# Optimization experiments

Hardware: AMD Instinct MI355X
Metric: run time of the kernel (lower is better)

Reference implementation:

```python
import jax, jax.numpy as jnp
import numpy as np
from jax.ops import segment_sum

B = 4096      # graphs per side (= batch of triples)
NPG = 32      # nodes per graph
N = B * NPG   # total nodes per batched graph
EPG = 128     # edges per graph
E = B * EPG   # total edges per batched graph
D = 256       # emb_dim
D4 = D // 4   # gnn1 out dim


def setup_inputs() -> dict:
    key = jax.random.key(0)
    ks = jax.random.split(key, 16)
    base = jnp.repeat(jnp.arange(B, dtype=jnp.int32) * NPG, EPG)  # graph offsets per edge
    def edges(k1, k2):
        s = base + jax.random.randint(k1, (E,), 0, NPG, dtype=jnp.int32)
        d = base + jax.random.randint(k2, (E,), 0, NPG, dtype=jnp.int32)
        return s, d
    subj_src, subj_dst = edges(ks[0], ks[1])
    obj_src, obj_dst = edges(ks[2], ks[3])
    node_graph_ids = jnp.repeat(jnp.arange(B, dtype=jnp.int32), NPG)
    # negative sampling indices (precomputed randomness, as in _sample_batch_negative_triples)
    head_or_tail = jax.random.randint(ks[4], (B,), 0, 2, dtype=jnp.int32)
    random_rows = jax.random.permutation(ks[5], B).astype(jnp.int32)
    ar = jnp.arange(B, dtype=jnp.int32)
    corrupt_hidx = jnp.where(head_or_tail == 1, random_rows, ar)
    corrupt_tidx = jnp.where(head_or_tail == 0, random_rows, ar)
    s = 0.02
    p = lambda k, sh: jax.random.normal(k, sh, dtype=jnp.float32) * s
    return {
        "subj_node_embs": jax.random.normal(ks[6], (N, D), dtype=jnp.float32),
        "obj_node_embs": jax.random.normal(ks[7], (N, D), dtype=jnp.float32),
        "rel_tok_embs": jax.random.normal(ks[8], (B, D), dtype=jnp.float32),
        "subj_src": subj_src, "subj_dst": subj_dst,
        "obj_src": obj_src, "obj_dst": obj_dst,
        "node_graph_ids": node_graph_ids,
        "corrupt_hidx": corrupt_hidx, "corrupt_tidx": corrupt_tidx,
        "WO1": p(ks[9], (D4, D)), "bO1": jnp.zeros((D4,), jnp.float32),
        "WI1": p(ks[10], (D4, D)), "bI1": jnp.zeros((D4,), jnp.float32),
        "WO2": p(ks[11], (D, D4)), "bO2": jnp.zeros((D,), jnp.float32),
        "WI2": p(ks[12], (D, D4)), "bI2": jnp.zeros((D,), jnp.float32),
        "relW": p(ks[13], (D, D)), "relb": jnp.zeros((D,), jnp.float32),
    }


def _mean_agg(h, idx_from, idx_to, n):
    # mean over edges (idx_from -> idx_to) of h[idx_from], per destination node; 0 for isolated
    deg = segment_sum(jnp.ones((idx_from.shape[0],), h.dtype), idx_to, num_segments=n)
    s = segment_sum(jnp.take(h, idx_from, axis=0), idx_to, num_segments=n)
    return s / jnp.maximum(deg, 1.0)[:, None]


def _compgcn(src, dst, h, WO, bO, WI, bI):
    n = h.shape[0]
    ho = _mean_agg(h, src, dst, n)   # forward graph: mean of in-neighbor sources
    hi = _mean_agg(h, dst, src, n)   # reversed graph: mean of out-neighbor targets
    return (ho @ WO.T + bO) + (hi @ WI.T + bI)


def _graph_emb(src, dst, node_embs, gids, WO1, bO1, WI1, bI1, WO2, bO2, WI2, bI2):
    hn = jax.nn.relu(_compgcn(src, dst, node_embs, WO1, bO1, WI1, bI1))
    hn = jax.nn.relu(_compgcn(src, dst, hn, WO2, bO2, WI2, bI2))
    # mean readout per graph
    cnt = segment_sum(jnp.ones((hn.shape[0],), hn.dtype), gids, num_segments=B)
    return segment_sum(hn, gids, num_segments=B) / cnt[:, None]


def _dist(h, r, t):
    return jnp.linalg.norm(h + r - t, ord=2, axis=1)


def reference(subj_node_embs, obj_node_embs, rel_tok_embs,
              subj_src, subj_dst, obj_src, obj_dst, node_graph_ids,
              corrupt_hidx, corrupt_tidx,
              WO1, bO1, WI1, bI1, WO2, bO2, WI2, bI2, relW, relb):
    h_embs = _graph_emb(subj_src, subj_dst, subj_node_embs, node_graph_ids,
                        WO1, bO1, WI1, bI1, WO2, bO2, WI2, bI2)
    t_embs = _graph_emb(obj_src, obj_dst, obj_node_embs, node_graph_ids,
                        WO1, bO1, WI1, bI1, WO2, bO2, WI2, bI2)
    r_embs = jax.nn.relu(rel_tok_embs @ relW.T + relb)
    pos_scores = _dist(h_embs, r_embs, t_embs)
    neg_scores = _dist(h_embs[corrupt_hidx], r_embs, t_embs[corrupt_tidx])
    return pos_scores, neg_scores
```

## Files before the change

### kernel.cpp

```cpp
#include <hip/hip_runtime.h>
#include <hip/hip_bf16.h>

#define BGR 4096
#define DIM 256
#define NGPB 4
#define HS  257

typedef __bf16 bf16x8 __attribute__((ext_vector_type(8)));
typedef __bf16 bf16x4 __attribute__((ext_vector_type(4)));
typedef float  f32x4  __attribute__((ext_vector_type(4)));

typedef const __attribute__((address_space(1))) unsigned int* gas_u32p;
typedef __attribute__((address_space(3))) unsigned int* las_u32p;

__device__ __forceinline__ unsigned short f2b(float f) {
  unsigned u = __builtin_bit_cast(unsigned, f);
  u = (u + 0x7FFFu + ((u >> 16) & 1u)) >> 16;
  return (unsigned short)u;
}

__device__ __forceinline__ bf16x8 cvt8(float4 a, float4 b) {
  bf16x8 r;
  r[0] = (__bf16)a.x; r[1] = (__bf16)a.y; r[2] = (__bf16)a.z; r[3] = (__bf16)a.w;
  r[4] = (__bf16)b.x; r[5] = (__bf16)b.y; r[6] = (__bf16)b.z; r[7] = (__bf16)b.w;
  return r;
}
__device__ __forceinline__ bf16x4 cvt4(f32x4 c) {
  bf16x4 r;
  r[0] = (__bf16)c[0]; r[1] = (__bf16)c[1]; r[2] = (__bf16)c[2]; r[3] = (__bf16)c[3];
  return r;
}

__global__ void wcvt_kernel(
    const float* __restrict__ WO1, const float* __restrict__ WI1,
    const float* __restrict__ WO2, const float* __restrict__ WI2,
    const float* __restrict__ bO1, const float* __restrict__ bI1,
    const float* __restrict__ bO2, const float* __restrict__ bI2,
    unsigned short* __restrict__ W1b, unsigned short* __restrict__ W2b,
    float* __restrict__ b1, float* __restrict__ b2)
{
  const int i = blockIdx.x * 256 + threadIdx.x;
  { int j = i >> 8, k = i & 255;
    float v = (j < 64) ? WO1[j * 256 + k] : WI1[(j - 64) * 256 + k];
    W1b[i] = f2b(v); }
  { int j = i >> 7, k = i & 127;
    float v = (k < 64) ? WO2[j * 64 + k] : WI2[j * 64 + (k - 64)];
    W2b[i] = f2b(v); }
  if (i < 64)  b1[i] = bO1[i] + bI1[i];
  if (i < 256) b2[i] = bO2[i] + bI2[i];
}

__global__ __launch_bounds__(256)
__attribute__((amdgpu_waves_per_eu(1, 2)))
void gemm0_kernel(
    const float* __restrict__ subj, const float* __restrict__ obj,
    const unsigned short* __restrict__ W1b, unsigned short* __restrict__ Yt)
{
  __shared__ __align__(16) float S[2][32 * 256];
  const int t = threadIdx.x, w = t >> 6, l = t & 63;
  const int ln16 = l & 15, kg = l >> 4;
  const int gid0 = blockIdx.x * NGPB;

  {
    const int gid = gid0;
    const float* Eg = ((gid >> 12) ? obj : subj) + (size_t)(gid & (BGR - 1)) * 32 * DIM;
    #pragma unroll
    for (int i = 0; i < 8; i++) {
      const int r = w * 8 + i;
      const float* src = Eg + r * 256 + ((l ^ (r & 7)) << 2);
      __builtin_amdgcn_global_load_lds((gas_u32p)(const void*)src,
                                       (las_u32p)(void*)(&S[0][r * 256]), 16, 0, 0);
    }
  }

  bf16x8 B0[8], B1[8];
  {
    const unsigned short* wb0 = W1b + ((2 * w) * 16 + ln16) * 256 + kg * 8;
    const unsigned short* wb1 = W1b + ((2 * w + 1) * 16 + ln16) * 256 + kg * 8;
    #pragma unroll
    for (int ks = 0; ks < 8; ks++) {
      B0[ks] = *(const bf16x8*)(wb0 + ks * 32);
      B1[ks] = *(const bf16x8*)(wb1 + ks * 32);
    }
  }
  __syncthreads();

  for (int g = 0; g < NGPB; g++) {
    if (g + 1 < NGPB) {
      const int gid = gid0 + g + 1;
      const float* Eg = ((gid >> 12) ? obj : subj) + (size_t)(gid & (BGR - 1)) * 32 * DIM;
      #pragma unroll
      for (int i = 0; i < 8; i++) {
        const int r = w * 8 + i;
        const float* src = Eg + r * 256 + ((l ^ (r & 7)) << 2);
        __builtin_amdgcn_global_load_lds((gas_u32p)(const void*)src,
                                         (las_u32p)(void*)(&S[(g + 1) & 1][r * 256]),
                                         16, 0, 0);
      }
    }

    const float* eb = &S[g & 1][0];
    const int swz = ln16 & 7;
    f32x4 a00 = {0,0,0,0}, a01 = {0,0,0,0}, a10 = {0,0,0,0}, a11 = {0,0,0,0};
    #pragma unroll
    for (int ks = 0; ks < 8; ks++) {
      const int c0 = ks * 8 + kg * 2;
      float4 lo0 = *(const float4*)(eb + ln16 * 256 + ((c0 ^ swz) << 2));
      float4 hi0 = *(const float4*)(eb + ln16 * 256 + (((c0 + 1) ^ swz) << 2));
      bf16x8 A0 = cvt8(lo0, hi0);
      a00 = __builtin_amdgcn_mfma_f32_16x16x32_bf16(A0, B0[ks], a00, 0, 0, 0);
      a01 = __builtin_amdgcn_mfma_f32_16x16x32_bf16(A0, B1[ks], a01, 0, 0, 0);
      float4 lo1 = *(const float4*)(eb + (16 + ln16) * 256 + ((c0 ^ swz) << 2));
      float4 hi1 = *(const float4*)(eb + (16 + ln16) * 256 + (((c0 + 1) ^ swz) << 2));
      bf16x8 A1 = cvt8(lo1, hi1);
      a10 = __builtin_amdgcn_mfma_f32_16x16x32_bf16(A1, B0[ks], a10, 0, 0, 0);
      a11 = __builtin_amdgcn_mfma_f32_16x16x32_bf16(A1, B1[ks], a11, 0, 0, 0);
    }
    {
      const int gid = gid0 + g;
      unsigned short* yo = Yt + (size_t)gid * 4096 + kg * 4;
      *(bf16x4*)(yo + ((2 * w) * 16 + ln16) * 32)          = cvt4(a00);
      *(bf16x4*)(yo + ((2 * w + 1) * 16 + ln16) * 32)      = cvt4(a01);
      *(bf16x4*)(yo + ((2 * w) * 16 + ln16) * 32 + 16)     = cvt4(a10);
      *(bf16x4*)(yo + ((2 * w + 1) * 16 + ln16) * 32 + 16) = cvt4(a11);
    }
    __syncthreads();
  }
}

__global__ __launch_bounds__(256)
__attribute__((amdgpu_waves_per_eu(2, 3)))
void graph_bc_kernel(
    const unsigned short* __restrict__ Yt,
    const int* __restrict__ ssrc, const int* __restrict__ sdst,
    const int* __restrict__ osrc, const int* __restrict__ odst,
    const unsigned short* __restrict__ W2b,
    const float* __restrict__ b1, const float* __restrict__ b2,
    float* __restrict__ gout)
{
  __shared__ __align__(16) unsigned char S[53248];
  const int t = threadIdx.x, w = t >> 6, l = t & 63;
  const int ln16 = l & 15, kg = l >> 4;
  const int gid = blockIdx.x * 4 + w;
  const int side = gid >> 12, g = gid & (BGR - 1);
  unsigned char* h1t = S + w * 13312;
  unsigned char* a2  = S + w * 13312 + 4608;
  unsigned* cw = (unsigned*)a2;

  const int* __restrict__ srcp = side ? osrc : ssrc;
  const int* __restrict__ dstp = side ? odst : sdst;

  const int eb = g * 128 + l;
  const int s0 = srcp[eb] & 31, s1 = srcp[eb + 64] & 31;
  const int d0 = dstp[eb] & 31, d1 = dstp[eb + 64] & 31;

  const unsigned short* yg = Yt + (size_t)gid * 4096;
  bf16x8 Bo[4], Bi[4];
  #pragma unroll
  for (int nt = 0; nt < 4; nt++) {
    Bo[nt] = *(const bf16x8*)(yg + (nt * 16 + ln16) * 32 + kg * 8);
    Bi[nt] = *(const bf16x8*)(yg + (64 + nt * 16 + ln16) * 32 + kg * 8);
  }
  float b1j[4];
  #pragma unroll
  for (int nt = 0; nt < 4; nt++) b1j[nt] = b1[nt * 16 + ln16];

  #pragma unroll
  for (int i = 0; i < 5; i++) cw[l + i * 64] = 0u;
  atomicAdd(&cw[d0 * 8 + (s0 >> 2)], 1u << ((s0 & 3) * 8));
  atomicAdd(&cw[d1 * 8 + (s1 >> 2)], 1u << ((s1 & 3) * 8));
  atomicAdd(&cw[256 + d0], 1u); atomicAdd(&cw[256 + d1], 1u);
  atomicAdd(&cw[288 + s0], 1u); atomicAdd(&cw[288 + s1], 1u);

  bf16x8 m1f[2], m2f[2];
  #pragma unroll
  for (int hf = 0; hf < 2; hf++) {
    const int r = hf * 16 + ln16;
    const float fi = 1.0f / fmaxf((float)cw[256 + r], 1.0f);
    const float fo = 1.0f / fmaxf((float)cw[288 + r], 1.0f);
    const unsigned w0 = cw[r * 8 + kg * 2], w1 = cw[r * 8 + kg * 2 + 1];
    bf16x8 a, b;
    #pragma unroll
    for (int q = 0; q < 4; q++) {
      a[q]     = (__bf16)((float)((w0 >> (q * 8)) & 255u) * fi);
      a[4 + q] = (__bf16)((float)((w1 >> (q * 8)) & 255u) * fi);
    }
    #pragma unroll
    for (int q = 0; q < 8; q++) {
      const unsigned wq = cw[(kg * 8 + q) * 8 + (r >> 2)];
      b[q] = (__bf16)((float)((wq >> ((r & 3) * 8)) & 255u) * fo);
    }
    m1f[hf] = a; m2f[hf] = b;
  }

  #pragma unroll
  for (int mt = 0; mt < 2; mt++)
    #pragma unroll
    for (int nt = 0; nt < 4; nt++) {
      f32x4 z = {0.f, 0.f, 0.f, 0.f};
      f32x4 c = __builtin_amdgcn_mfma_f32_16x16x32_bf16(m1f[mt], Bo[nt], z, 0, 0, 0);
      c = __builtin_amdgcn_mfma_f32_16x16x32_bf16(m2f[mt], Bi[nt], c, 0, 0, 0);
      f32x4 hv = { fmaxf(c[0] + b1j[nt], 0.f), fmaxf(c[1] + b1j[nt], 0.f),
                   fmaxf(c[2] + b1j[nt], 0.f), fmaxf(c[3] + b1j[nt], 0.f) };
      *(bf16x4*)(h1t + (nt * 16 + ln16) * 72 + (mt * 16 + kg * 4) * 2) = cvt4(hv);
    }

  #pragma unroll
  for (int mta = 0; mta < 4; mta++) {
    bf16x8 Af = *(const bf16x8*)(h1t + (mta * 16 + ln16) * 72 + kg * 16);
    #pragma unroll
    for (int hf = 0; hf < 2; hf++)
      #pragma unroll
      for (int ntd = 0; ntd < 2; ntd++) {
        f32x4 z = {0.f, 0.f, 0.f, 0.f};
        f32x4 c = __builtin_amdgcn_mfma_f32_16x16x32_bf16(
            Af, hf ? m2f[ntd] : m1f[ntd], z, 0, 0, 0);
        *(bf16x4*)(a2 + (ntd * 16 + ln16) * 272 + hf * 128 + mta * 32 + kg * 8) = cvt4(c);
      }
  }

  bf16x8 BF[2][4];
  #pragma unroll
  for (int ntd = 0; ntd < 2; ntd++)
    #pragma unroll
    for (int ks = 0; ks < 4; ks++)
      BF[ntd][ks] = *(const bf16x8*)(a2 + (ntd * 16 + ln16) * 272 + ks * 64 + kg * 16);

  #pragma unroll
  for (int mt = 0; mt < 16; mt++) {
    bf16x8 AW[4];
    #pragma unroll
    for (int ks = 0; ks < 4; ks++)
      AW[ks] = *(const bf16x8*)(W2b + (mt * 16 + ln16) * 128 + ks * 32 + kg * 8);
    f32x4 a0 = {0.f, 0.f, 0.f, 0.f}, a1 = {0.f, 0.f, 0.f, 0.f};
    #pragma unroll
    for (int ks = 0; ks < 4; ks++) {
      a0 = __builtin_amdgcn_mfma_f32_16x16x32_bf16(AW[ks], BF[0][ks], a0, 0, 0, 0);
      a1 = __builtin_amdgcn_mfma_f32_16x16x32_bf16(AW[ks], BF[1][ks], a1, 0, 0, 0);
    }
    const float4 bb = *(const float4*)(b2 + mt * 16 + kg * 4);
    float v0 = fmaxf(a0[0] + bb.x, 0.f) + fmaxf(a1[0] + bb.x, 0.f);
    float v1 = fmaxf(a0[1] + bb.y, 0.f) + fmaxf(a1[1] + bb.y, 0.f);
    float v2 = fmaxf(a0[2] + bb.z, 0.f) + fmaxf(a1[2] + bb.z, 0.f);
    float v3 = fmaxf(a0[3] + bb.w, 0.f) + fmaxf(a1[3] + bb.w, 0.f);
    #pragma unroll
    for (int d = 1; d < 16; d <<= 1) {
      v0 += __shfl_xor(v0, d); v1 += __shfl_xor(v1, d);
      v2 += __shfl_xor(v2, d); v3 += __shfl_xor(v3, d);
    }
    if (ln16 == 0) {
      float4 o = { v0 * 0.03125f, v1 * 0.03125f, v2 * 0.03125f, v3 * 0.03125f };
      *(float4*)(gout + (size_t)gid * DIM + mt * 16 + kg * 4) = o;
    }
  }
}

__global__ __launch_bounds__(256, 4) void rel_kernel(
    const float* __restrict__ rel, const float* __restrict__ relW,
    const float* __restrict__ relb, float* __restrict__ r_out)
{
  __shared__ float srel[16 * HS];
  const int t = threadIdx.x;
  const int b0 = blockIdx.x << 4;
  #pragma unroll
  for (int i = 0; i < 4; i++) {
    int f = (i << 8) + t;
    int r = f >> 6, k4 = f & 63;
    float4 x = *(const float4*)(rel + (size_t)(b0 + r) * DIM + (k4 << 2));
    float* d = &srel[r * HS + (k4 << 2)];
    d[0] = x.x; d[1] = x.y; d[2] = x.z; d[3] = x.w;
  }
  __syncthreads();
  const int r = t & 15, jg = t >> 4;
  const float* pa = &srel[r * HS];
  const float* w = relW + (size_t)(jg * 16) * DIM;
  float acc[16];
  #pragma unroll
  for (int jj = 0; jj < 16; jj++) acc[jj] = 0.f;
  for (int k0 = 0; k0 < DIM; k0 += 16) {
    float a[16];
    #pragma unroll
    for (int u = 0; u < 16; u++) a[u] = pa[k0 + u];
    #pragma unroll
    for (int jj = 0; jj < 16; jj++) {
      const float* wr = w + jj * DIM + k0;
      #pragma unroll
      for (int u = 0; u < 16; u += 4) {
        float4 wv = *(const float4*)(wr + u);
        acc[jj] += a[u]*wv.x + a[u+1]*wv.y + a[u+2]*wv.z + a[u+3]*wv.w;
      }
    }
  }
  float* outp = r_out + (size_t)(b0 + r) * DIM + jg * 16;
  #pragma unroll
  for (int jj = 0; jj < 16; jj++) outp[jj] = fmaxf(acc[jj] + relb[jg * 16 + jj], 0.f);
}

__global__ __launch_bounds__(256) void dist_kernel(
    const float* __restrict__ hemb, const float* __restrict__ temb,
    const float* __restrict__ remb, const int* __restrict__ chx,
    const int* __restrict__ ctx, float* __restrict__ out)
{
  const int t = threadIdx.x;
  const int w = t >> 6, l = t & 63;
  const int b = (blockIdx.x << 2) + w;
  float4 h4 = *(const float4*)(hemb + (size_t)b * DIM + (l << 2));
  float4 r4 = *(const float4*)(remb + (size_t)b * DIM + (l << 2));
  float4 t4 = *(const float4*)(temb + (size_t)b * DIM + (l << 2));
  int hb = chx[b], tb = ctx[b];
  float4 hn = *(const float4*)(hemb + (size_t)hb * DIM + (l << 2));
  float4 tn = *(const float4*)(temb + (size_t)tb * DIM + (l << 2));
  float x0 = h4.x + r4.x - t4.x, x1 = h4.y + r4.y - t4.y;
  float x2 = h4.z + r4.z - t4.z, x3 = h4.w + r4.w - t4.w;
  float dp = x0*x0 + x1*x1 + x2*x2 + x3*x3;
  float y0 = hn.x + r4.x - tn.x, y1 = hn.y + r4.y - tn.y;
  float y2 = hn.z + r4.z - tn.z, y3 = hn.w + r4.w - tn.w;
  float dn = y0*y0 + y1*y1 + y2*y2 + y3*y3;
  #pragma unroll
  for (int off = 32; off >= 1; off >>= 1) {
    dp += __shfl_down(dp, off);
    dn += __shfl_down(dn, off);
  }
  if (l == 0) {
    out[b] = sqrtf(dp);
    out[BGR + b] = sqrtf(dn);
  }
}

extern "C" void kernel_launch(void* const* d_in, const int* in_sizes, int n_in,
                              void* d_out, int out_size, void* d_ws, size_t ws_size,
                              hipStream_t stream) {
  const float* subj_embs = (const float*)d_in[0];
  const float* obj_embs  = (const float*)d_in[1];
  const float* rel_tok   = (const float*)d_in[2];
  const int* subj_src = (const int*)d_in[3];
  const int* subj_dst = (const int*)d_in[4];
  const int* obj_src  = (const int*)d_in[5];
  const int* obj_dst  = (const int*)d_in[6];
  const int* chx = (const int*)d_in[8];
  const int* ctx = (const int*)d_in[9];
  const float* WO1 = (const float*)d_in[10];
  const float* bO1 = (const float*)d_in[11];
  const float* WI1 = (const float*)d_in[12];
  const float* bI1 = (const float*)d_in[13];
  const float* WO2 = (const float*)d_in[14];
  const float* bO2 = (const float*)d_in[15];
  const float* WI2 = (const float*)d_in[16];
  const float* bI2 = (const float*)d_in[17];
  const float* relW = (const float*)d_in[18];
  const float* relb = (const float*)d_in[19];

  float* g_embs = (float*)d_ws;
  float* r_embs = g_embs + (size_t)2 * BGR * DIM;
  unsigned short* W1b = (unsigned short*)((char*)d_ws + 12582912);
  unsigned short* W2b = W1b + 32768;
  float* b1 = (float*)((char*)d_ws + 12713984);
  float* b2 = b1 + 64;
  unsigned short* Yt = (unsigned short*)((char*)d_ws + 16777216);
  float* out = (float*)d_out;

  wcvt_kernel<<<128, 256, 0, stream>>>(WO1, WI1, WO2, WI2, bO1, bI1, bO2, bI2,
                                       W1b, W2b, b1, b2);
  gemm0_kernel<<<2048, 256, 0, stream>>>(subj_embs, obj_embs, W1b, Yt);
  graph_bc_kernel<<<2048, 256, 0, stream>>>(
      Yt, subj_src, subj_dst, obj_src, obj_dst, W2b, b1, b2, g_embs);
  rel_kernel<<<BGR / 16, 256, 0, stream>>>(rel_tok, relW, relb, r_embs);
  dist_kernel<<<BGR / 4, 256, 0, stream>>>(
      g_embs, g_embs + (size_t)BGR * DIM, r_embs, chx, ctx, out);
}
```

Before: 221.0 us.

## Deepen gemm0 prefetch pipeline with explicit vmcnt waits and double graphs per block

Restructures the gemm0 staging loop so the next graph's async global-to-LDS load is issued two iterations ahead, with manual s_waitcnt vmcnt and raw s_barrier instead of __syncthreads. The aim is to overlap the memory stream with compute better. It also doubles graphs per block to amortize the weight register loads, halving the grid. The swizzle simplification (r&7 == i) is equivalent. Risks are fewer blocks for latency hiding and fragile manual waitcnt counts.

```diff
diff --git a/kernel.cpp b/kernel.cpp
--- a/kernel.cpp
+++ b/kernel.cpp
@@ -3,7 +3,7 @@
 
 #define BGR 4096
 #define DIM 256
-#define NGPB 4
+#define NGPB 8
 #define HS  257
 
 typedef __bf16 bf16x8 __attribute__((ext_vector_type(8)));
@@ -61,18 +61,19 @@
   const int ln16 = l & 15, kg = l >> 4;
   const int gid0 = blockIdx.x * NGPB;
 
-  {
-    const int gid = gid0;
+  auto STAGE = [&](int g, int buf) {
+    const int gid = gid0 + g;
     const float* Eg = ((gid >> 12) ? obj : subj) + (size_t)(gid & (BGR - 1)) * 32 * DIM;
     #pragma unroll
     for (int i = 0; i < 8; i++) {
       const int r = w * 8 + i;
-      const float* src = Eg + r * 256 + ((l ^ (r & 7)) << 2);
+      const float* src = Eg + r * 256 + ((l ^ i) << 2);
       __builtin_amdgcn_global_load_lds((gas_u32p)(const void*)src,
-                                       (las_u32p)(void*)(&S[0][r * 256]), 16, 0, 0);
-    }
-  }
-
+                                       (las_u32p)(void*)(&S[buf][r * 256]), 16, 0, 0);
+    }
+  };
+
+  STAGE(0, 0);
   bf16x8 B0[8], B1[8];
   {
     const unsigned short* wb0 = W1b + ((2 * w) * 16 + ln16) * 256 + kg * 8;
@@ -83,21 +84,14 @@
       B1[ks] = *(const bf16x8*)(wb1 + ks * 32);
     }
   }
-  __syncthreads();
-
+  STAGE(1, 1);
+
+  #pragma unroll
   for (int g = 0; g < NGPB; g++) {
-    if (g + 1 < NGPB) {
-      const int gid = gid0 + g + 1;
-      const float* Eg = ((gid >> 12) ? obj : subj) + (size_t)(gid & (BGR - 1)) * 32 * DIM;
-      #pragma unroll
-      for (int i = 0; i < 8; i++) {
-        const int r = w * 8 + i;
-        const float* src = Eg + r * 256 + ((l ^ (r & 7)) << 2);
-        __builtin_amdgcn_global_load_lds((gas_u32p)(const void*)src,
-                                         (las_u32p)(void*)(&S[(g + 1) & 1][r * 256]),
-                                         16, 0, 0);
-      }
-    }
+    if (g + 1 < NGPB) { asm volatile("s_waitcnt vmcnt(8)" ::: "memory"); }
+    else              { asm volatile("s_waitcnt vmcnt(0)" ::: "memory"); }
+    __builtin_amdgcn_s_barrier();
+    __builtin_amdgcn_sched_barrier(0);
 
     const float* eb = &S[g & 1][0];
     const int swz = ln16 & 7;
@@ -124,7 +118,11 @@
       *(bf16x4*)(yo + ((2 * w) * 16 + ln16) * 32 + 16)     = cvt4(a10);
       *(bf16x4*)(yo + ((2 * w + 1) * 16 + ln16) * 32 + 16) = cvt4(a11);
     }
-    __syncthreads();
+
+    __builtin_amdgcn_sched_barrier(0);
+    __builtin_amdgcn_s_barrier();
+    __builtin_amdgcn_sched_barrier(0);
+    if (g + 2 < NGPB) STAGE(g + 2, g & 1);
   }
 }
 
@@ -361,7 +359,7 @@
 
   wcvt_kernel<<<128, 256, 0, stream>>>(WO1, WI1, WO2, WI2, bO1, bI1, bO2, bI2,
                                        W1b, W2b, b1, b2);
-  gemm0_kernel<<<2048, 256, 0, stream>>>(subj_embs, obj_embs, W1b, Yt);
+  gemm0_kernel<<<1024, 256, 0, stream>>>(subj_embs, obj_embs, W1b, Yt);
   graph_bc_kernel<<<2048, 256, 0, stream>>>(
       Yt, subj_src, subj_dst, obj_src, obj_dst, W2b, b1, b2, g_embs);
   rel_kernel<<<BGR / 16, 256, 0, stream>>>(rel_tok, relW, relb, r_embs);
```

Measured after the change: 217.3 us. No clear change (-1.7%).
